# Performance work log

Measured on AMD Instinct MI355X. Metric: run time of the kernel, lower is better.

## Reference

```python
import jax, jax.numpy as jnp
import numpy as np


def setup_inputs() -> dict:
    key = jax.random.key(0)
    k1, k2, k3 = jax.random.split(key, 3)
    N, E, C, OUT = 100000, 1000000, 64, 64
    x = jax.random.normal(k1, (N, C), dtype=jnp.float32)
    edge_index = jax.random.randint(k2, (2, E), 0, N, dtype=jnp.int32)
    W = jax.random.normal(k3, (2 * C, OUT), dtype=jnp.float32) * (1.0 / np.sqrt(2 * C))
    b = jnp.zeros((OUT,), dtype=jnp.float32)
    return {"x": x, "edge_index": edge_index, "W": W, "b": b}


def reference(x, edge_index, W, b):
    # MRConv: x_j = scatter_max(x[src] - x[dst], dst); out = relu(cat([x, x_j]) @ W + b)
    N = x.shape[0]
    src, dst = edge_index[0], edge_index[1]
    diff = x[src] - x[dst]                                  # [E, C] gather + diff
    x_j = jax.ops.segment_max(diff, dst, num_segments=N)    # [N, C] scatter-max
    # nodes with no incoming edges get -inf from segment_max; tg fills them with 0
    x_j = jnp.where(jnp.isfinite(x_j), x_j, 0.0)
    h = jnp.concatenate([x, x_j], axis=1)                   # [N, 2C]
    return jax.nn.relu(h @ W + b)                           # [N, OUT]
```

## Files before the change

### kernel.cpp

```cpp
#include <hip/hip_runtime.h>
#include <math.h>

#define SENT 0x007FFFFFu
#define NEGINF_BITS 0xFF800000u
#define NA 256
#define SB_SHIFT 6
#define SB_MASK ((1u << SB_SHIFT) - 1u)
#define NB 64
#define PITCH 68
#define MAXSB 2048

typedef __attribute__((ext_vector_type(8))) short bf16x8;
typedef __attribute__((ext_vector_type(4))) float f32x4;

__device__ __forceinline__ unsigned int fmap(float f) {
    unsigned int u = __float_as_uint(f);
    return (u & 0x80000000u) ? ~u : (u | 0x80000000u);
}
__device__ __forceinline__ unsigned int fmap_bits(unsigned int u) {
    return (u & 0x80000000u) ? ~u : (u | 0x80000000u);
}
__device__ __forceinline__ float funmap(unsigned int u) {
    unsigned int bits = (u & 0x80000000u) ? (u ^ 0x80000000u) : ~u;
    return __uint_as_float(bits);
}
__device__ __forceinline__ unsigned short tobf(float f) {
    unsigned int u = __float_as_uint(f);
    u += 0x7FFFu + ((u >> 16) & 1u);
    return (unsigned short)(u >> 16);
}
__device__ __forceinline__ float frombf(unsigned short s) {
    return __uint_as_float((unsigned int)s << 16);
}

__global__ void __launch_bounds__(256) cast_kernel(const float* __restrict__ x,
                                                   unsigned short* __restrict__ xb,
                                                   long long n) {
    long long i = ((long long)blockIdx.x * blockDim.x + threadIdx.x) * 8;
    long long stride = (long long)gridDim.x * blockDim.x * 8;
    for (; i < n; i += stride) {
        float4 a = *(const float4*)(x + i);
        float4 c = *(const float4*)(x + i + 4);
        uint4 o;
        o.x = (unsigned)tobf(a.x) | ((unsigned)tobf(a.y) << 16);
        o.y = (unsigned)tobf(a.z) | ((unsigned)tobf(a.w) << 16);
        o.z = (unsigned)tobf(c.x) | ((unsigned)tobf(c.y) << 16);
        o.w = (unsigned)tobf(c.z) | ((unsigned)tobf(c.w) << 16);
        *(uint4*)(xb + i) = o;
    }
}


__global__ void __launch_bounds__(256) histA_kernel(const int* __restrict__ ei,
                                                    unsigned* __restrict__ counts2,
                                                    int E, int nsb, int chunk) {
    __shared__ unsigned h[MAXSB];
    for (int t = threadIdx.x; t < nsb; t += 256) h[t] = 0u;
    __syncthreads();
    int beg = blockIdx.x * chunk;
    int end = min(beg + chunk, E);
    for (int i = beg + threadIdx.x; i < end; i += 256)
        atomicAdd(&h[((unsigned)ei[E + i]) >> SB_SHIFT], 1u);
    __syncthreads();
    for (int t = threadIdx.x; t < nsb; t += 256)
        counts2[(size_t)t * NA + blockIdx.x] = h[t];
}

__global__ void __launch_bounds__(512) rowscan_kernel(unsigned* __restrict__ counts2,
                                                      unsigned* __restrict__ sbtot, int nsb) {
    int lane = threadIdx.x & 63;
    int sb = blockIdx.x * 8 + (threadIdx.x >> 6);
    if (sb >= nsb) return;
    unsigned* row = counts2 + (size_t)sb * NA;
    uint4 v = *(const uint4*)(row + 4 * lane);
    unsigned local = v.x + v.y + v.z + v.w;
    unsigned incl = local;
    #pragma unroll
    for (int d = 1; d < 64; d <<= 1) {
        unsigned t = __shfl_up(incl, d);
        if (lane >= d) incl += t;
    }
    unsigned e0 = incl - local;
    uint4 o;
    o.x = e0;
    o.y = e0 + v.x;
    o.z = o.y + v.y;
    o.w = o.z + v.z;
    *(uint4*)(row + 4 * lane) = o;
    if (lane == 63) sbtot[sb] = incl;
}

__global__ void __launch_bounds__(1024) sbscan_kernel(const unsigned* __restrict__ sbtot,
                                                      unsigned* __restrict__ sbbase, int nsb) {
    __shared__ unsigned s[1024];
    __shared__ unsigned carry_s;
    if (threadIdx.x == 0) carry_s = 0u;
    __syncthreads();
    for (int chunk = 0; chunk < nsb; chunk += 1024) {
        int i = chunk + threadIdx.x;
        unsigned v = (i < nsb) ? sbtot[i] : 0u;
        s[threadIdx.x] = v;
        __syncthreads();
        for (int d = 1; d < 1024; d <<= 1) {
            unsigned t = (threadIdx.x >= d) ? s[threadIdx.x - d] : 0u;
            __syncthreads();
            s[threadIdx.x] += t;
            __syncthreads();
        }
        unsigned carry = carry_s;
        if (i < nsb) sbbase[i] = carry + s[threadIdx.x] - v;
        __syncthreads();
        if (threadIdx.x == 1023) carry_s = carry + s[1023];
        __syncthreads();
    }
    if (threadIdx.x == 0) sbbase[nsb] = carry_s;
}

__global__ void __launch_bounds__(256) placeB_kernel(const int* __restrict__ ei,
                                                     const unsigned* __restrict__ counts2,
                                                     const unsigned* __restrict__ sbbase,
                                                     unsigned* __restrict__ ssrc,
                                                     int E, int nsb, int chunk) {
    __shared__ unsigned fill[MAXSB];
    for (int t = threadIdx.x; t < nsb; t += 256)
        fill[t] = sbbase[t] + counts2[(size_t)t * NA + blockIdx.x];
    __syncthreads();
    int beg = blockIdx.x * chunk;
    int end = min(beg + chunk, E);
    for (int i = beg + threadIdx.x; i < end; i += 256) {
        unsigned src = (unsigned)ei[i];
        unsigned dst = (unsigned)ei[E + i];
        unsigned pos = atomicAdd(&fill[dst >> SB_SHIFT], 1u);
        ssrc[pos] = (src << SB_SHIFT) | (dst & SB_MASK);
    }
}

__global__ void __launch_bounds__(256, 6) reduceBf_kernel(const unsigned short* __restrict__ xb,
                                                          const unsigned* __restrict__ sbbase,
                                                          const unsigned* __restrict__ ssrc,
                                                          unsigned short* __restrict__ xj, int N) {
    __shared__ unsigned M[NB * PITCH];
    int tid = threadIdx.x;
    int lane = tid & 63;
    int wid = tid >> 6;

    for (int i = tid; i < NB * PITCH; i += 256) M[i] = SENT;

    int nodeBase = blockIdx.x * NB;
    int beg = (int)sbbase[blockIdx.x];
    int end = (int)sbbase[blockIdx.x + 1];
    __syncthreads();

    for (int i0 = beg + wid * 64; i0 < end; i0 += 256) {
        int i = i0 + lane;
        unsigned p = (i < end) ? ssrc[i] : 0u;
        int cnt = min(64, end - i0);
        unsigned pfirst = __shfl(p, 0);
        for (int j = 0; j < cnt; j += 16) {
            unsigned pp[16];
            unsigned uu[16];
            #pragma unroll
            for (int k = 0; k < 16; ++k) {
                pp[k] = (j + k < cnt) ? __shfl(p, j + k) : pfirst;
                uu[k] = (unsigned)xb[(size_t)(pp[k] >> SB_SHIFT) * 64 + lane] << 16;
            }
            #pragma unroll
            for (int k = 0; k < 16; ++k)
                atomicMax(&M[(pp[k] & SB_MASK) * PITCH + lane], fmap_bits(uu[k]));
        }
    }
    __syncthreads();

    for (int row = wid; row < NB; row += 4) {
        int n = nodeBase + row;
        if (n < N) {
            unsigned um = M[row * PITCH + lane];
            unsigned short o = 0;
            if (um != SENT) {
                float mx = funmap(um);
                float xv = frombf(xb[(size_t)n * 64 + lane]);
                o = tobf(mx - xv);
            }
            xj[(size_t)n * 64 + lane] = o;
        }
    }
}

__global__ void __launch_bounds__(256) mlpBf_kernel(const unsigned short* __restrict__ xb,
                                                    const unsigned short* __restrict__ xj,
                                                    const float* __restrict__ W,
                                                    const float* __restrict__ b,
                                                    float* __restrict__ out, int N) {
    int lane = threadIdx.x & 63;
    int wid  = threadIdx.x >> 6;
    int r = lane & 15;
    int g = lane >> 4;

    bf16x8 Bf[4][4];
    #pragma unroll
    for (int nt = 0; nt < 4; ++nt)
        #pragma unroll
        for (int kt = 0; kt < 4; ++kt) {
            const float* wp = W + (size_t)(kt * 32 + g * 8) * 64 + nt * 16 + r;
            bf16x8 f;
            #pragma unroll
            for (int j = 0; j < 8; ++j) f[j] = (short)tobf(wp[(size_t)j * 64]);
            Bf[nt][kt] = f;
        }
    float bias[4];
    #pragma unroll
    for (int nt = 0; nt < 4; ++nt) bias[nt] = b[nt * 16 + r];

    int nTiles = (N + 15) >> 4;
    int totalWaves = gridDim.x * 4;
    for (int tile = blockIdx.x * 4 + wid; tile < nTiles; tile += totalWaves) {
        int nodeBase = tile << 4;
        int rowIdx = min(nodeBase + r, N - 1);
        const unsigned short* xp = xb + (size_t)rowIdx * 64;
        const unsigned short* jp = xj + (size_t)rowIdx * 64;

        bf16x8 Af[4];
        #pragma unroll
        for (int kt = 0; kt < 2; ++kt) {
            Af[kt]     = *(const bf16x8*)(xp + kt * 32 + g * 8);
            Af[2 + kt] = *(const bf16x8*)(jp + kt * 32 + g * 8);
        }

        f32x4 acc[4];
        #pragma unroll
        for (int nt = 0; nt < 4; ++nt) {
            f32x4 a = {bias[nt], bias[nt], bias[nt], bias[nt]};
            acc[nt] = a;
        }
        #pragma unroll
        for (int nt = 0; nt < 4; ++nt)
            #pragma unroll
            for (int kt = 0; kt < 4; ++kt)
                acc[nt] = __builtin_amdgcn_mfma_f32_16x16x32_bf16(Af[kt], Bf[nt][kt], acc[nt], 0, 0, 0);

        #pragma unroll
        for (int nt = 0; nt < 4; ++nt)
            #pragma unroll
            for (int reg = 0; reg < 4; ++reg) {
                int nrow = nodeBase + g * 4 + reg;
                if (nrow < N)
                    out[(size_t)nrow * 64 + nt * 16 + r] = fmaxf(acc[nt][reg], 0.0f);
            }
    }
}


__global__ void __launch_bounds__(256, 6) reduceB_kernel(const float* __restrict__ x,
                                                         const unsigned* __restrict__ sbbase,
                                                         const unsigned* __restrict__ ssrc,
                                                         float* __restrict__ xj, int N) {
    __shared__ unsigned M[NB * PITCH];
    int tid = threadIdx.x;
    int lane = tid & 63;
    int wid = tid >> 6;

    for (int i = tid; i < NB * PITCH; i += 256) M[i] = SENT;

    int nodeBase = blockIdx.x * NB;
    int beg = (int)sbbase[blockIdx.x];
    int end = (int)sbbase[blockIdx.x + 1];
    __syncthreads();

    for (int i0 = beg + wid * 64; i0 < end; i0 += 256) {
        int i = i0 + lane;
        unsigned p = (i < end) ? ssrc[i] : 0u;
        int cnt = min(64, end - i0);
        unsigned pfirst = __shfl(p, 0);
        for (int j = 0; j < cnt; j += 16) {
            unsigned pp[16];
            float vv[16];
            #pragma unroll
            for (int k = 0; k < 16; ++k) {
                pp[k] = (j + k < cnt) ? __shfl(p, j + k) : pfirst;
                vv[k] = x[(size_t)(pp[k] >> SB_SHIFT) * 64 + lane];
            }
            #pragma unroll
            for (int k = 0; k < 16; ++k)
                atomicMax(&M[(pp[k] & SB_MASK) * PITCH + lane], fmap(vv[k]));
        }
    }
    __syncthreads();

    for (int row = wid; row < NB; row += 4) {
        int n = nodeBase + row;
        if (n < N) xj[(size_t)n * 64 + lane] = funmap(M[row * PITCH + lane]);
    }
}

template <bool MAPPED>
__global__ void __launch_bounds__(256) mlp_kernel(const float* __restrict__ x,
                                                  const unsigned int* xj,
                                                  const float* __restrict__ W,
                                                  const float* __restrict__ b,
                                                  float* out, int N) {
    int lane = threadIdx.x & 63;
    int wid  = threadIdx.x >> 6;
    int r = lane & 15;
    int g = lane >> 4;

    bf16x8 Bf[4][4];
    #pragma unroll
    for (int nt = 0; nt < 4; ++nt)
        #pragma unroll
        for (int kt = 0; kt < 4; ++kt) {
            const float* wp = W + (size_t)(kt * 32 + g * 8) * 64 + nt * 16 + r;
            bf16x8 f;
            #pragma unroll
            for (int j = 0; j < 8; ++j) f[j] = (short)tobf(wp[(size_t)j * 64]);
            Bf[nt][kt] = f;
        }
    float bias[4];
    #pragma unroll
    for (int nt = 0; nt < 4; ++nt) bias[nt] = b[nt * 16 + r];

    int nTiles = (N + 15) >> 4;
    int totalWaves = gridDim.x * 4;
    for (int tile = blockIdx.x * 4 + wid; tile < nTiles; tile += totalWaves) {
        int nodeBase = tile << 4;
        int rowIdx = min(nodeBase + r, N - 1);
        const float* xp = x + (size_t)rowIdx * 64;
        const unsigned int* jp = xj + (size_t)rowIdx * 64;

        bf16x8 Af[4];
        float xs[2][8];
        #pragma unroll
        for (int kt = 0; kt < 2; ++kt) {
            float4 flo = *(const float4*)(xp + kt * 32 + g * 8);
            float4 fhi = *(const float4*)(xp + kt * 32 + g * 8 + 4);
            xs[kt][0] = flo.x; xs[kt][1] = flo.y; xs[kt][2] = flo.z; xs[kt][3] = flo.w;
            xs[kt][4] = fhi.x; xs[kt][5] = fhi.y; xs[kt][6] = fhi.z; xs[kt][7] = fhi.w;
            bf16x8 f;
            #pragma unroll
            for (int j = 0; j < 8; ++j) f[j] = (short)tobf(xs[kt][j]);
            Af[kt] = f;
        }
        #pragma unroll
        for (int kt = 0; kt < 2; ++kt) {
            uint4 ulo = *(const uint4*)(jp + kt * 32 + g * 8);
            uint4 uhi = *(const uint4*)(jp + kt * 32 + g * 8 + 4);
            unsigned int uu[8] = {ulo.x, ulo.y, ulo.z, ulo.w, uhi.x, uhi.y, uhi.z, uhi.w};
            bf16x8 f;
            #pragma unroll
            for (int j = 0; j < 8; ++j) {
                bool empty;
                float v;
                if (MAPPED) { empty = (uu[j] == SENT); v = funmap(uu[j]); }
                else        { empty = (uu[j] == NEGINF_BITS); v = __uint_as_float(uu[j]); }
                f[j] = (short)tobf(empty ? 0.0f : (v - xs[kt][j]));
            }
            Af[2 + kt] = f;
        }

        f32x4 acc[4];
        #pragma unroll
        for (int nt = 0; nt < 4; ++nt) {
            f32x4 a = {bias[nt], bias[nt], bias[nt], bias[nt]};
            acc[nt] = a;
        }
        #pragma unroll
        for (int nt = 0; nt < 4; ++nt)
            #pragma unroll
            for (int kt = 0; kt < 4; ++kt)
                acc[nt] = __builtin_amdgcn_mfma_f32_16x16x32_bf16(Af[kt], Bf[nt][kt], acc[nt], 0, 0, 0);

        #pragma unroll
        for (int nt = 0; nt < 4; ++nt)
            #pragma unroll
            for (int reg = 0; reg < 4; ++reg) {
                int nrow = nodeBase + g * 4 + reg;
                if (nrow < N)
                    out[(size_t)nrow * 64 + nt * 16 + r] = fmaxf(acc[nt][reg], 0.0f);
            }
    }
}


__global__ void init_kernel(uint4* __restrict__ ws, int n4) {
    int i = blockIdx.x * blockDim.x + threadIdx.x;
    int stride = gridDim.x * blockDim.x;
    uint4 v = make_uint4(SENT, SENT, SENT, SENT);
    for (; i < n4; i += stride) ws[i] = v;
}

__global__ void scatter_kernel(const float* __restrict__ x,
                               const int* __restrict__ ei,
                               unsigned int* __restrict__ ws, int E) {
    long long gid = (long long)blockIdx.x * blockDim.x + threadIdx.x;
    int e = (int)(gid >> 6);
    int lane = (int)(gid & 63);
    if (e >= E) return;
    int src = ei[e];
    int dst = ei[E + e];
    unsigned int m = fmap(x[(size_t)src * 64 + lane]);
    unsigned int* p = ws + (size_t)dst * 64 + lane;
    if (m > *p) atomicMax(p, m);
}

extern "C" void kernel_launch(void* const* d_in, const int* in_sizes, int n_in,
                              void* d_out, int out_size, void* d_ws, size_t ws_size,
                              hipStream_t stream) {
    const float* x  = (const float*)d_in[0];
    const int*   ei = (const int*)d_in[1];
    const float* W  = (const float*)d_in[2];
    const float* b  = (const float*)d_in[3];
    float* out = (float*)d_out;

    int N = in_sizes[0] / 64;
    int E = in_sizes[1] / 2;

    int nsb = (N + NB - 1) >> SB_SHIFT;
    int chunk = (E + NA - 1) / NA;

    size_t counts2_b = (size_t)nsb * NA * 4;
    size_t sbtot_b   = (size_t)((nsb + 63) & ~63) * 4;
    size_t sbbase_b  = (size_t)(nsb + 1 + 63) / 64 * 64 * 4;
    size_t ssrc_b    = (size_t)E * 4;
    size_t xb_b      = (size_t)N * 64 * 2;
    size_t xjb_b     = (size_t)N * 64 * 2;
    size_t xj32_b    = (size_t)N * 64 * 4;
    size_t needB     = counts2_b + sbtot_b + sbbase_b + ssrc_b;
    size_t needA     = needB + xb_b + xjb_b;

    if (ws_size >= needA && nsb <= MAXSB) {
        char* p = (char*)d_ws;
        unsigned* counts2 = (unsigned*)p; p += counts2_b;
        unsigned* sbtot   = (unsigned*)p; p += sbtot_b;
        unsigned* sbbase  = (unsigned*)p; p += sbbase_b;
        unsigned* ssrc    = (unsigned*)p; p += ssrc_b;
        unsigned short* xb  = (unsigned short*)p; p += xb_b;
        unsigned short* xjb = (unsigned short*)p;

        long long n = (long long)N * 64;
        int cgrid = (int)((n / 8 + 255) / 256);
        cast_kernel<<<cgrid, 256, 0, stream>>>(x, xb, n);
        histA_kernel<<<NA, 256, 0, stream>>>(ei, counts2, E, nsb, chunk);
        rowscan_kernel<<<(nsb + 7) / 8, 512, 0, stream>>>(counts2, sbtot, nsb);
        sbscan_kernel<<<1, 1024, 0, stream>>>(sbtot, sbbase, nsb);
        placeB_kernel<<<NA, 256, 0, stream>>>(ei, counts2, sbbase, ssrc, E, nsb, chunk);
        reduceBf_kernel<<<nsb, 256, 0, stream>>>(xb, sbbase, ssrc, xjb, N);
        mlpBf_kernel<<<782, 256, 0, stream>>>(xb, xjb, W, b, out, N);
    } else if (ws_size >= needB && nsb <= MAXSB) {
        char* p = (char*)d_ws;
        unsigned* counts2 = (unsigned*)p; p += counts2_b;
        unsigned* sbtot   = (unsigned*)p; p += sbtot_b;
        unsigned* sbbase  = (unsigned*)p; p += sbbase_b;
        unsigned* ssrc    = (unsigned*)p; p += ssrc_b;
        float* xjp = (ws_size >= needB + xj32_b) ? (float*)p : (float*)d_out;

        histA_kernel<<<NA, 256, 0, stream>>>(ei, counts2, E, nsb, chunk);
        rowscan_kernel<<<(nsb + 7) / 8, 512, 0, stream>>>(counts2, sbtot, nsb);
        sbscan_kernel<<<1, 1024, 0, stream>>>(sbtot, sbbase, nsb);
        placeB_kernel<<<NA, 256, 0, stream>>>(ei, counts2, sbbase, ssrc, E, nsb, chunk);
        reduceB_kernel<<<nsb, 256, 0, stream>>>(x, sbbase, ssrc, xjp, N);
        mlp_kernel<false><<<782, 256, 0, stream>>>(x, (const unsigned*)xjp, W, b, out, N);
    } else {
        size_t need2 = (size_t)N * 64 * 4;
        unsigned int* scratch = (ws_size >= need2) ? (unsigned int*)d_ws : (unsigned int*)d_out;
        init_kernel<<<2048, 256, 0, stream>>>((uint4*)scratch, N * 16);
        long long sthreads = (long long)E * 64;
        int sblocks = (int)((sthreads + 255) / 256);
        scatter_kernel<<<sblocks, 256, 0, stream>>>(x, ei, scratch, E);
        mlp_kernel<true><<<782, 256, 0, stream>>>(x, scratch, W, b, out, N);
    }
}
```

Before: 99.94 us.

## Fuse cast and histogram kernels, halve super-bucket size, tweak launch configs

Merges the bf16 cast and the destination histogram into one launch, with block-index ranges picking the role, to cut one kernel launch and let the two independent jobs overlap. Super-bucket size drops from 64 to 32 nodes, which doubles the number of reduce blocks for better load balance but adds more scan work and a larger counts array. Also removes the occupancy hint from the reduce kernels, makes the edge-list load in the reduce nontemporal, and derives the MLP grid size from N instead of a constant.

```diff
diff --git a/kernel.cpp b/kernel.cpp
--- a/kernel.cpp
+++ b/kernel.cpp
@@ -4,11 +4,12 @@
 #define SENT 0x007FFFFFu
 #define NEGINF_BITS 0xFF800000u
 #define NA 256
-#define SB_SHIFT 6
+#define SB_SHIFT 5
 #define SB_MASK ((1u << SB_SHIFT) - 1u)
-#define NB 64
+#define NB 32
 #define PITCH 68
-#define MAXSB 2048
+#define MAXSB 4096
+#define CGRID 1024
 
 typedef __attribute__((ext_vector_type(8))) short bf16x8;
 typedef __attribute__((ext_vector_type(4))) float f32x4;
@@ -33,23 +34,39 @@
     return __uint_as_float((unsigned int)s << 16);
 }
 
-__global__ void __launch_bounds__(256) cast_kernel(const float* __restrict__ x,
-                                                   unsigned short* __restrict__ xb,
-                                                   long long n) {
-    long long i = ((long long)blockIdx.x * blockDim.x + threadIdx.x) * 8;
-    long long stride = (long long)gridDim.x * blockDim.x * 8;
-    for (; i < n; i += stride) {
-        float4 a = *(const float4*)(x + i);
-        float4 c = *(const float4*)(x + i + 4);
-        uint4 o;
-        o.x = (unsigned)tobf(a.x) | ((unsigned)tobf(a.y) << 16);
-        o.y = (unsigned)tobf(a.z) | ((unsigned)tobf(a.w) << 16);
-        o.z = (unsigned)tobf(c.x) | ((unsigned)tobf(c.y) << 16);
-        o.w = (unsigned)tobf(c.z) | ((unsigned)tobf(c.w) << 16);
-        *(uint4*)(xb + i) = o;
-    }
-}
-
+__global__ void __launch_bounds__(256) casthist_kernel(const float* __restrict__ x,
+                                                       unsigned short* __restrict__ xb,
+                                                       long long n,
+                                                       const int* __restrict__ ei,
+                                                       unsigned* __restrict__ counts2,
+                                                       int E, int nsb, int chunk, int cgrid) {
+    __shared__ unsigned h[MAXSB];
+    if ((int)blockIdx.x < cgrid) {
+        long long i = ((long long)blockIdx.x * 256 + threadIdx.x) * 8;
+        long long stride = (long long)cgrid * 256 * 8;
+        for (; i < n; i += stride) {
+            float4 a = *(const float4*)(x + i);
+            float4 c = *(const float4*)(x + i + 4);
+            uint4 o;
+            o.x = (unsigned)tobf(a.x) | ((unsigned)tobf(a.y) << 16);
+            o.y = (unsigned)tobf(a.z) | ((unsigned)tobf(a.w) << 16);
+            o.z = (unsigned)tobf(c.x) | ((unsigned)tobf(c.y) << 16);
+            o.w = (unsigned)tobf(c.z) | ((unsigned)tobf(c.w) << 16);
+            *(uint4*)(xb + i) = o;
+        }
+    } else {
+        int hb = (int)blockIdx.x - cgrid;
+        for (int t = threadIdx.x; t < nsb; t += 256) h[t] = 0u;
+        __syncthreads();
+        int beg = hb * chunk;
+        int end = min(beg + chunk, E);
+        for (int i = beg + threadIdx.x; i < end; i += 256)
+            atomicAdd(&h[((unsigned)ei[E + i]) >> SB_SHIFT], 1u);
+        __syncthreads();
+        for (int t = threadIdx.x; t < nsb; t += 256)
+            counts2[(size_t)t * NA + hb] = h[t];
+    }
+}
 
 __global__ void __launch_bounds__(256) histA_kernel(const int* __restrict__ ei,
                                                     unsigned* __restrict__ counts2,
@@ -135,10 +152,10 @@
     }
 }
 
-__global__ void __launch_bounds__(256, 6) reduceBf_kernel(const unsigned short* __restrict__ xb,
-                                                          const unsigned* __restrict__ sbbase,
-                                                          const unsigned* __restrict__ ssrc,
-                                                          unsigned short* __restrict__ xj, int N) {
+__global__ void __launch_bounds__(256) reduceBf_kernel(const unsigned short* __restrict__ xb,
+                                                       const unsigned* __restrict__ sbbase,
+                                                       const unsigned* __restrict__ ssrc,
+                                                       unsigned short* __restrict__ xj, int N) {
     __shared__ unsigned M[NB * PITCH];
     int tid = threadIdx.x;
     int lane = tid & 63;
@@ -153,7 +170,7 @@
 
     for (int i0 = beg + wid * 64; i0 < end; i0 += 256) {
         int i = i0 + lane;
-        unsigned p = (i < end) ? ssrc[i] : 0u;
+        unsigned p = (i < end) ? __builtin_nontemporal_load(&ssrc[i]) : 0u;
         int cnt = min(64, end - i0);
         unsigned pfirst = __shfl(p, 0);
         for (int j = 0; j < cnt; j += 16) {
@@ -250,10 +267,10 @@
 }
 
 
-__global__ void __launch_bounds__(256, 6) reduceB_kernel(const float* __restrict__ x,
-                                                         const unsigned* __restrict__ sbbase,
-                                                         const unsigned* __restrict__ ssrc,
-                                                         float* __restrict__ xj, int N) {
+__global__ void __launch_bounds__(256) reduceB_kernel(const float* __restrict__ x,
+                                                      const unsigned* __restrict__ sbbase,
+                                                      const unsigned* __restrict__ ssrc,
+                                                      float* __restrict__ xj, int N) {
     __shared__ unsigned M[NB * PITCH];
     int tid = threadIdx.x;
     int lane = tid & 63;
@@ -426,6 +443,8 @@
     size_t needB     = counts2_b + sbtot_b + sbbase_b + ssrc_b;
     size_t needA     = needB + xb_b + xjb_b;
 
+    int mgrid = (((N + 15) >> 4) + 3) / 4;
+
     if (ws_size >= needA && nsb <= MAXSB) {
         char* p = (char*)d_ws;
         unsigned* counts2 = (unsigned*)p; p += counts2_b;
@@ -436,14 +455,12 @@
         unsigned short* xjb = (unsigned short*)p;
 
         long long n = (long long)N * 64;
-        int cgrid = (int)((n / 8 + 255) / 256);
-        cast_kernel<<<cgrid, 256, 0, stream>>>(x, xb, n);
-        histA_kernel<<<NA, 256, 0, stream>>>(ei, counts2, E, nsb, chunk);
+        casthist_kernel<<<CGRID + NA, 256, 0, stream>>>(x, xb, n, ei, counts2, E, nsb, chunk, CGRID);
         rowscan_kernel<<<(nsb + 7) / 8, 512, 0, stream>>>(counts2, sbtot, nsb);
         sbscan_kernel<<<1, 1024, 0, stream>>>(sbtot, sbbase, nsb);
         placeB_kernel<<<NA, 256, 0, stream>>>(ei, counts2, sbbase, ssrc, E, nsb, chunk);
         reduceBf_kernel<<<nsb, 256, 0, stream>>>(xb, sbbase, ssrc, xjb, N);
-        mlpBf_kernel<<<782, 256, 0, stream>>>(xb, xjb, W, b, out, N);
+        mlpBf_kernel<<<mgrid, 256, 0, stream>>>(xb, xjb, W, b, out, N);
     } else if (ws_size >= needB && nsb <= MAXSB) {
         char* p = (char*)d_ws;
         unsigned* counts2 = (unsigned*)p; p += counts2_b;
@@ -457,7 +474,7 @@
         sbscan_kernel<<<1, 1024, 0, stream>>>(sbtot, sbbase, nsb);
         placeB_kernel<<<NA, 256, 0, stream>>>(ei, counts2, sbbase, ssrc, E, nsb, chunk);
         reduceB_kernel<<<nsb, 256, 0, stream>>>(x, sbbase, ssrc, xjp, N);
-        mlp_kernel<false><<<782, 256, 0, stream>>>(x, (const unsigned*)xjp, W, b, out, N);
+        mlp_kernel<false><<<mgrid, 256, 0, stream>>>(x, (const unsigned*)xjp, W, b, out, N);
     } else {
         size_t need2 = (size_t)N * 64 * 4;
         unsigned int* scratch = (ws_size >= need2) ? (unsigned int*)d_ws : (unsigned int*)d_out;
@@ -465,6 +482,6 @@
         long long sthreads = (long long)E * 64;
         int sblocks = (int)((sthreads + 255) / 256);
         scatter_kernel<<<sblocks, 256, 0, stream>>>(x, ei, scratch, E);
-        mlp_kernel<true><<<782, 256, 0, stream>>>(x, scratch, W, b, out, N);
-    }
-}
+        mlp_kernel<true><<<mgrid, 256, 0, stream>>>(x, scratch, W, b, out, N);
+    }
+}
```

Result: slower. 104.1 us (+4.2%).
